# Kernel tuning notes

Hardware: AMD Instinct MI355X
Metric: run time of the kernel (lower is better)

## Reference

```python
import jax, jax.numpy as jnp
import numpy as np

NQ, NT, BSZ, E, NH = 100, 197, 128, 768, 12
HD = E // NH
EPS = 1e-12  # torch F.normalize default eps


def _l2norm(x, axis=-1):
    n = jnp.linalg.norm(x, axis=axis, keepdims=True)
    return x / jnp.maximum(n, EPS)


def setup_inputs() -> dict:
    rng = jax.random.key(0)
    ks = jax.random.split(rng, 10)
    s = 0.02  # xavier-ish scale for weights
    return {
        "query": jax.random.normal(ks[0], (NQ, BSZ, E), jnp.float32),
        "key": jax.random.normal(ks[1], (NT, BSZ, E), jnp.float32),
        "value": jax.random.normal(ks[2], (NT, BSZ, E), jnp.float32),
        "in_proj_weight": jax.random.normal(ks[3], (3 * E, E), jnp.float32) * s,
        "in_proj_bias": jnp.zeros((3 * E,), jnp.float32),
        "out_proj_weight": jax.random.normal(ks[4], (E, E), jnp.float32) * s,
        "out_proj_bias": jnp.zeros((E,), jnp.float32),
        "temperature": jnp.ones((NH, 1, 1), jnp.float32),
        "q_mapper": jax.random.normal(ks[5], (1, NT, NQ), jnp.float32),
        "x_mapper": jax.random.normal(ks[6], (1, NQ, NT), jnp.float32),
    }


def reference(query, key, value, in_proj_weight, in_proj_bias,
              out_proj_weight, out_proj_bias, temperature, q_mapper, x_mapper):
    nq, bsz, e = query.shape
    nt = key.shape[0]
    # packed in-projection: split into q/k/v weights
    wq, wk, wv = jnp.split(in_proj_weight, 3, axis=0)
    bq, bk, bv = jnp.split(in_proj_bias, 3, axis=0)
    q = query @ wq.T + bq   # [Nq, bsz, E]
    k = key @ wk.T + bk     # [Nt, bsz, E]
    v = value @ wv.T + bv   # [Nt, bsz, E]
    # reshape to [bsz, nh, hd, N] (channel-major for cross-covariance attn)
    q = q.reshape(nq, bsz, NH, HD).transpose(1, 2, 3, 0)  # [b, h, d, Nq]
    k = k.reshape(nt, bsz, NH, HD).transpose(1, 2, 3, 0)  # [b, h, d, Nt]
    v = v.reshape(nt, bsz, NH, HD).transpose(1, 2, 3, 0)  # [b, h, d, Nt]
    # normalize channel vectors over tokens
    qn = _l2norm(q)
    kn = _l2norm(k)
    # mappers: normalize over last dim, then shape to [Nq, Nt] operators
    qm_op = _l2norm(q_mapper[0])  # [Nt, Nq] normalized over Nq; transpose below
    xm_op = _l2norm(x_mapper[0])  # [Nq, Nt] normalized over Nt
    # qm = q @ q_mapper^T : [b,h,d,Nq] x [Nq,Nt] -> [b,h,d,Nt]
    qm = jnp.einsum('bhdq,tq->bhdt', qn, qm_op)
    # cross-covariance attention over channels: [b,h,d,d]
    attn = jnp.einsum('bhdt,bhet->bhde', qm, kn) * temperature[None]  # temp [nh,1,1] broadcasts per-head
    attn = jax.nn.softmax(attn, axis=-1)
    x = jnp.einsum('bhde,bhet->bhdt', attn, v)        # [b,h,d,Nt]
    out = jnp.einsum('bhdt,qt->bhdq', x, xm_op)       # [b,h,d,Nq]
    # back to [Nq, bsz, E]
    out = out.transpose(3, 0, 1, 2).reshape(nq, bsz, e)
    out = out @ out_proj_weight.T + out_proj_bias
    return out
```

## Files before the change

### kernel.cpp

```cpp
#include <hip/hip_runtime.h>
#include <hip/hip_bf16.h>

using bf16 = __hip_bfloat16;

constexpr int NQ  = 100;
constexpr int NT  = 197;
constexpr int BSZ = 128;
constexpr int EMB = 768;
constexpr int NHD = 12;
constexpr int HDD = 64;
constexpr int COLS = BSZ * EMB;
constexpr int M_Q  = 12800;
constexpr int M_KV = 25216;
constexpr int M_KVP = 25344;
constexpr int TPAD = 224;

constexpr size_t SZ_Q16  = (size_t)M_Q  * EMB * 2;
constexpr size_t SZ_KV16 = (size_t)M_KV * EMB * 2;
constexpr size_t SZ_KVP  = (size_t)M_KVP * EMB * 2;
constexpr size_t SZ_WI   = (size_t)3 * EMB * EMB * 2;
constexpr size_t SZ_T16  = (size_t)COLS * TPAD * 2;
constexpr size_t OFF_QB   = 256;
constexpr size_t OFF_KB   = OFF_QB + SZ_Q16;
constexpr size_t OFF_VB   = OFF_KB + SZ_KV16;
constexpr size_t OFF_WI   = OFF_VB + SZ_KV16;
constexpr size_t OFF_QP16 = OFF_WI + SZ_WI;
constexpr size_t OFF_KP16 = OFF_QP16 + SZ_Q16;
constexpr size_t OFF_VP16 = OFF_KP16 + SZ_KVP;
constexpr size_t OFF_QMNT = OFF_VP16 + SZ_KVP;
constexpr size_t OFF_XMNT = OFF_QMNT + 57344;
constexpr size_t OFF_WO   = OFF_XMNT + 57344;
constexpr size_t OFF_KPT  = 256;
constexpr size_t OFF_VPT  = OFF_KPT + SZ_T16;
constexpr size_t OFF_W16T = OFF_VPT + SZ_T16;
constexpr size_t OFF_QNT  = OFF_KP16;
constexpr size_t OFF_G16  = OFF_VP16;
constexpr size_t OFF_XO   = 256;

__device__ __forceinline__ float dl(const float* p) { return *p; }
__device__ __forceinline__ float dl(const bf16* p) { return __bfloat162float(*p); }

__device__ __forceinline__ ushort f2bf(float x) {
    union { float f; unsigned u; } v; v.f = x;
    unsigned r = v.u + 0x7FFFu + ((v.u >> 16) & 1u);
    return (ushort)(r >> 16);
}
__device__ __forceinline__ float bf2f(ushort x) {
    union { unsigned u; float f; } v; v.u = (unsigned)x << 16;
    return v.f;
}
__device__ __forceinline__ void dstore(float* p, float v) { *p = v; }
__device__ __forceinline__ void dstore(bf16* p, float v) { *p = __float2bfloat16(v); }

typedef __attribute__((ext_vector_type(8))) short short8;
typedef __attribute__((ext_vector_type(4))) short shortv4;
typedef __attribute__((ext_vector_type(4))) float f32x4;

__device__ __forceinline__ void gload16(const bf16* g, ushort* l) {
    __builtin_amdgcn_global_load_lds(
        (const __attribute__((address_space(1))) unsigned int*)g,
        (__attribute__((address_space(3))) unsigned int*)l, 16, 0, 0);
}

__device__ __forceinline__ int2 xcd_swz(int bx, int by, int gx, int gy) {
    const int nwg = gx * gy;
    const int L = by * gx + bx;
    const int q = nwg >> 3, r = nwg & 7;
    const int c = L & 7, i = L >> 3;
    const int wg = (c < r ? c * (q + 1) : r * (q + 1) + (c - r) * q) + i;
    return make_int2(wg % gx, wg / gx);
}

__global__ __launch_bounds__(256) void k_cvt5(
        const float* __restrict__ s0, bf16* __restrict__ d0,
        const float* __restrict__ s1, bf16* __restrict__ d1,
        const float* __restrict__ s2, bf16* __restrict__ d2,
        const float* __restrict__ s3, bf16* __restrict__ d3,
        const float* __restrict__ s4, bf16* __restrict__ d4) {
    int bk = blockIdx.x;
    const float* s; bf16* d; int lb;
    if      (bk < 864)   { s = s0; d = d0; lb = bk; }
    else if (bk < 5664)  { s = s1; d = d1; lb = bk - 864; }
    else if (bk < 15120) { s = s2; d = d2; lb = bk - 5664; }
    else if (bk < 24576) { s = s3; d = d3; lb = bk - 15120; }
    else                 { s = s4; d = d4; lb = bk - 24576; }
    size_t i = ((size_t)lb * 256 + threadIdx.x) * 8;
    float4 a = *(const float4*)(s + i), b = *(const float4*)(s + i + 4);
    short8 r;
    r[0] = (short)f2bf(a.x); r[1] = (short)f2bf(a.y); r[2] = (short)f2bf(a.z); r[3] = (short)f2bf(a.w);
    r[4] = (short)f2bf(b.x); r[5] = (short)f2bf(b.y); r[6] = (short)f2bf(b.z); r[7] = (short)f2bf(b.w);
    *(short8*)(d + i) = r;
}

template <typename T>
__global__ __launch_bounds__(128) void k_qmn(const T* qm, bf16* dstT) {
    __shared__ float red[128];
    int t = blockIdx.x, q = threadIdx.x;
    float v = (t < NT && q < NQ) ? dl(&qm[t * NQ + q]) : 0.f;
    red[q] = v * v;
    __syncthreads();
    for (int s = 64; s > 0; s >>= 1) { if (q < s) red[q] += red[q + s]; __syncthreads(); }
    float inv = 1.f / fmaxf(sqrtf(red[0]), 1e-12f);
    dstore(&dstT[(size_t)q * TPAD + t], (t < NT && q < NQ) ? v * inv : 0.f);
}

template <typename T>
__global__ __launch_bounds__(256) void k_xmn(const T* xm, bf16* dstT) {
    __shared__ float red[256];
    int q = blockIdx.x, t = threadIdx.x;
    float v = (q < NQ && t < NT) ? dl(&xm[q * NT + t]) : 0.f;
    red[t] = v * v;
    __syncthreads();
    for (int s = 128; s > 0; s >>= 1) { if (t < s) red[t] += red[t + s]; __syncthreads(); }
    float inv = 1.f / fmaxf(sqrtf(red[0]), 1e-12f);
    if (t < TPAD) dstore(&dstT[(size_t)q * TPAD + t], (q < NQ && t < NT) ? v * inv : 0.f);
}

template <int NR, int TP, int NORM>
__global__ __launch_bounds__(256) void k_trn(const bf16* __restrict__ src,
        bf16* __restrict__ dst) {
    __shared__ ushort tile[TP * 73];
    __shared__ float ssp[4][64];
    __shared__ float inv_s[64];
    const int col0 = blockIdx.x * 64;
    const int tid = threadIdx.x;
    const int c = tid & 63, tb = tid >> 6;
    float ss = 0.f;
#pragma unroll
    for (int it = 0; it < TP / 4; ++it) {
        int t = tb + it * 4;
        ushort v = 0;
        if (t < NR) v = *(const ushort*)&src[(size_t)t * COLS + col0 + c];
        tile[t * 73 + c] = v;
        if (NORM) { float f = bf2f(v); ss = fmaf(f, f, ss); }
    }
    if (NORM) {
        ssp[tb][c] = ss;
        __syncthreads();
        if (tid < 64) {
            float s = ssp[0][tid] + ssp[1][tid] + ssp[2][tid] + ssp[3][tid];
            inv_s[tid] = 1.f / fmaxf(sqrtf(s), 1e-12f);
        }
    }
    __syncthreads();
    constexpr int UPC = TP / 8;
#pragma unroll
    for (int it = 0; it < (64 * UPC) / 256; ++it) {
        int u = tid + it * 256;
        int cc = u / UPC, t0 = (u % UPC) * 8;
        float inv = NORM ? inv_s[cc] : 1.f;
        short8 s;
#pragma unroll
        for (int r = 0; r < 8; ++r) {
            ushort raw = tile[(t0 + r) * 73 + cc];
            s[r] = NORM ? (short)f2bf(bf2f(raw) * inv) : (short)raw;
        }
        *(short8*)&dst[(size_t)(col0 + cc) * TP + t0] = s;
    }
}

__global__ __launch_bounds__(256) void k_trn2(const bf16* __restrict__ kp,
        const bf16* __restrict__ vp, bf16* __restrict__ kpT, bf16* __restrict__ vpT) {
    __shared__ ushort tile[TPAD * 73];
    __shared__ float ssp[4][64];
    __shared__ float inv_s[64];
    const int bk = blockIdx.x;
    const bool vseg = bk >= 1536;
    const bf16* src = vseg ? vp : kp;
    bf16* dst = vseg ? vpT : kpT;
    const int col0 = (vseg ? bk - 1536 : bk) * 64;
    const int tid = threadIdx.x;
    const int c = tid & 63, tb = tid >> 6;
    float ss = 0.f;
#pragma unroll
    for (int it = 0; it < TPAD / 4; ++it) {
        int t = tb + it * 4;
        ushort v = 0;
        if (t < NT) v = *(const ushort*)&src[(size_t)t * COLS + col0 + c];
        tile[t * 73 + c] = v;
        if (!vseg) { float f = bf2f(v); ss = fmaf(f, f, ss); }
    }
    if (!vseg) {
        ssp[tb][c] = ss;
        __syncthreads();
        if (tid < 64) {
            float s = ssp[0][tid] + ssp[1][tid] + ssp[2][tid] + ssp[3][tid];
            inv_s[tid] = 1.f / fmaxf(sqrtf(s), 1e-12f);
        }
    }
    __syncthreads();
    constexpr int UPC = TPAD / 8;
#pragma unroll
    for (int it = 0; it < (64 * UPC) / 256; ++it) {
        int u = tid + it * 256;
        int cc = u / UPC, t0 = (u % UPC) * 8;
        float inv = vseg ? 1.f : inv_s[cc];
        short8 s;
#pragma unroll
        for (int r = 0; r < 8; ++r) {
            ushort raw = tile[(t0 + r) * 73 + cc];
            s[r] = vseg ? (short)raw : (short)f2bf(bf2f(raw) * inv);
        }
        *(short8*)&dst[(size_t)(col0 + cc) * TPAD + t0] = s;
    }
}

#define MM8_BAR  { __builtin_amdgcn_s_barrier(); __builtin_amdgcn_sched_barrier(0); }
#define MM8_LGK0 { asm volatile("s_waitcnt lgkmcnt(0)" ::: "memory"); __builtin_amdgcn_sched_barrier(0); }
#define MM8_VM8  { asm volatile("s_waitcnt vmcnt(8)" ::: "memory"); __builtin_amdgcn_sched_barrier(0); }
#define MM8_VM0  { asm volatile("s_waitcnt vmcnt(0)" ::: "memory"); __builtin_amdgcn_sched_barrier(0); }
#define MM8_STAGE(CUR, ISB, H, KT) do { \
    const bf16* gb_ = (ISB) ? (Wb + (size_t)(n0 + (H)*128 + srow) * EMB + (KT)*64 + sk_sw) \
                            : (Ab + (size_t)(m0 + (H)*128 + srow) * EMB + (KT)*64 + sk_sw); \
    ushort* lb_ = ((ISB) ? B_lds : A_lds) + (CUR)*16384 + (H)*8192 + wid*512; \
    gload16(gb_, lb_); \
    gload16(gb_ + (size_t)64 * EMB, lb_ + 4096); \
} while (0)
#define MM8_LOADFRAGS(CUR, KK, AARR, BARR) { \
    _Pragma("unroll") for (int m_ = 0; m_ < 8; ++m_) { \
        int ra_ = wr*128 + m_*16 + ln15; \
        AARR[m_] = *(const short8*)&A_lds[(CUR)*16384 + ra_*64 + ((((KK)*4 + q8) ^ (ra_ & 7)))*8]; } \
    _Pragma("unroll") for (int j_ = 0; j_ < 4; ++j_) { \
        int rb_ = wc*64 + j_*16 + ln15; \
        BARR[j_] = *(const short8*)&B_lds[(CUR)*16384 + rb_*64 + ((((KK)*4 + q8) ^ (rb_ & 7)))*8]; } }
#define MM8_QUAD(AARR, BARR, MB) { \
    __builtin_amdgcn_s_setprio(1); \
    _Pragma("unroll") for (int m_ = 0; m_ < 4; ++m_) \
        _Pragma("unroll") for (int j_ = 0; j_ < 4; ++j_) \
            acc[(MB) + m_][j_] = __builtin_amdgcn_mfma_f32_16x16x32_bf16( \
                AARR[(MB) + m_], BARR[j_], acc[(MB) + m_][j_], 0, 0, 0); \
    __builtin_amdgcn_s_setprio(0); }

__global__ __launch_bounds__(512, 2) void k_mm8(
        const bf16* __restrict__ A0, const bf16* __restrict__ A1, const bf16* __restrict__ A2,
        const bf16* __restrict__ W,
        bf16* __restrict__ C0, bf16* __restrict__ C1, bf16* __restrict__ C2,
        const float* __restrict__ bias, int mt0, int mt01) {
    __shared__ __align__(16) ushort A_lds[2 * 16384];
    __shared__ __align__(16) ushort B_lds[2 * 16384];
    const int tid = threadIdx.x;
    const int2 bxy = xcd_swz(blockIdx.x, blockIdx.y, gridDim.x, gridDim.y);
    int seg = 0, lby = bxy.y;
    if (bxy.y < mt0)       { seg = 0; lby = bxy.y; }
    else if (bxy.y < mt01) { seg = 1; lby = bxy.y - mt0; }
    else                   { seg = 2; lby = bxy.y - mt01; }
    const bf16* Ab = seg == 0 ? A0 : (seg == 1 ? A1 : A2);
    const bf16* Wb = W + (size_t)seg * EMB * EMB;
    bf16* C = seg == 0 ? C0 : (seg == 1 ? C1 : C2);
    const float* bp = bias + seg * EMB;
    const int m0 = lby * 256, n0 = bxy.x * 256;
    const int wid = tid >> 6, ln = tid & 63;
    const int wr = wid >> 2, wc = wid & 3;
    const int ln15 = ln & 15, q8 = ln >> 4;
    const int srow = tid >> 3;
    const int sk_sw = (((tid & 7) ^ (srow & 7)) * 8);

    f32x4 acc[8][4] = {};
    short8 a0[8], b0[4], a1[8], b1[4];

    MM8_STAGE(0, 0, 0, 0); MM8_STAGE(0, 0, 1, 0); MM8_STAGE(0, 1, 0, 0); MM8_STAGE(0, 1, 1, 0);
    MM8_STAGE(1, 0, 0, 1); MM8_STAGE(1, 0, 1, 1); MM8_STAGE(1, 1, 0, 1); MM8_STAGE(1, 1, 1, 1);
    MM8_VM8;
    MM8_BAR;

    for (int t = 0; t < 12; ++t) {
        const int c = t & 1, nxt = t + 2;
        MM8_LOADFRAGS(c, 0, a0, b0);
        MM8_QUAD(a0, b0, 0);
        MM8_BAR;
        MM8_LOADFRAGS(c, 1, a1, b1);
        MM8_QUAD(a0, b0, 4);
        MM8_LGK0;
        MM8_BAR;
        if (nxt < 12) { MM8_STAGE(c, 0, 0, nxt); MM8_STAGE(c, 0, 1, nxt); }
        MM8_QUAD(a1, b1, 0);
        MM8_BAR;
        if (nxt < 12) { MM8_STAGE(c, 1, 0, nxt); MM8_STAGE(c, 1, 1, nxt); }
        if (t < 10) { MM8_VM8; } else { MM8_VM0; }
        MM8_QUAD(a1, b1, 4);
        MM8_BAR;
    }

#pragma unroll
    for (int j = 0; j < 4; ++j) {
        const int n = n0 + wc * 64 + j * 16 + ln15;
        const float bv = bp[n];
#pragma unroll
        for (int m = 0; m < 8; ++m) {
            const int mb = m0 + wr * 128 + m * 16 + q8 * 4;
#pragma unroll
            for (int r = 0; r < 4; ++r)
                dstore(&C[(size_t)(mb + r) * EMB + n], acc[m][j][r] + bv);
        }
    }
}

template <typename TBias>
__global__ __launch_bounds__(256) void k_proj2(
        const bf16* __restrict__ Aq, const bf16* __restrict__ Ak, const bf16* __restrict__ Av,
        const bf16* __restrict__ Wi, bf16* __restrict__ Cq, bf16* __restrict__ Ck,
        bf16* __restrict__ Cv, const TBias* __restrict__ bias) {
    __shared__ __align__(16) ushort As[128 * 32];
    __shared__ __align__(16) ushort Bs[128 * 32];
    const int t = threadIdx.x;
    const int2 bxy = xcd_swz(blockIdx.x, blockIdx.y, gridDim.x, gridDim.y);
    int byy = bxy.y, seg, lby;
    if (byy < 100)      { seg = 0; lby = byy; }
    else if (byy < 297) { seg = 1; lby = byy - 100; }
    else                { seg = 2; lby = byy - 297; }
    const bf16* Ab = seg == 0 ? Aq : (seg == 1 ? Ak : Av);
    const bf16* Wb = Wi + (size_t)seg * EMB * EMB;
    bf16* C = seg == 0 ? Cq : (seg == 1 ? Ck : Cv);
    const TBias* bp = bias + seg * EMB;
    const int n0 = bxy.x * 128, m0 = lby * 128;
    const int ln = t & 63, wv = t >> 6;
    const int ln15 = ln & 15, q8 = ln >> 4;
    const int mw = (wv & 1) * 64, nw = (wv >> 1) * 64;
    const int sr = ln >> 2, sk = (ln & 3) * 8;
    const bf16* gA = Ab + (size_t)(m0 + wv * 32 + sr) * EMB + sk;
    const bf16* gB = Wb + (size_t)(n0 + wv * 32 + sr) * EMB + sk;
    const size_t r16 = (size_t)16 * EMB;
    ushort* lA = &As[wv * 1024];
    ushort* lB = &Bs[wv * 1024];
    f32x4 acc[4][4] = {};
    for (int k0 = 0; k0 < EMB; k0 += 32) {
        gload16(gA + k0,       lA);
        gload16(gA + r16 + k0, lA + 512);
        gload16(gB + k0,       lB);
        gload16(gB + r16 + k0, lB + 512);
        __syncthreads();
        short8 a[4], b[4];
#pragma unroll
        for (int i = 0; i < 4; ++i)
            a[i] = *(const short8*)&As[(mw + i * 16 + ln15) * 32 + q8 * 8];
#pragma unroll
        for (int j = 0; j < 4; ++j)
            b[j] = *(const short8*)&Bs[(nw + j * 16 + ln15) * 32 + q8 * 8];
#pragma unroll
        for (int i = 0; i < 4; ++i)
#pragma unroll
            for (int j = 0; j < 4; ++j)
                acc[i][j] = __builtin_amdgcn_mfma_f32_16x16x32_bf16(a[i], b[j], acc[i][j], 0, 0, 0);
        __syncthreads();
    }
#pragma unroll
    for (int j = 0; j < 4; ++j) {
        const int n = n0 + nw + j * 16 + ln15;
        const float bv = dl(&bp[n]);
#pragma unroll
        for (int i = 0; i < 4; ++i) {
            const int mb = m0 + mw + i * 16 + q8 * 4;
#pragma unroll
            for (int r = 0; r < 4; ++r)
                dstore(&C[(size_t)(mb + r) * EMB + n], acc[i][j][r] + bv);
        }
    }
}

__global__ __launch_bounds__(256) void k_gw(
        const bf16* __restrict__ kpT, const bf16* __restrict__ vpT,
        const bf16* __restrict__ qmnT, const bf16* __restrict__ xmnT,
        bf16* __restrict__ g16, bf16* __restrict__ w16T) {
    __shared__ __align__(16) ushort As[128 * 32];
    __shared__ __align__(16) ushort Bs[128 * 32];
    const int t = threadIdx.x;
    const int2 bxy = xcd_swz(blockIdx.x, blockIdx.y, gridDim.x, gridDim.y);
    const bool wseg = bxy.y >= 768;
    const int lby = wseg ? bxy.y - 768 : bxy.y;
    const bf16* Ab = wseg ? vpT : kpT;
    const bf16* Bb = wseg ? xmnT : qmnT;
    const int m0 = lby * 128;
    const int ln = t & 63, wv = t >> 6;
    const int ln15 = ln & 15, q8 = ln >> 4;
    const int mw = (wv & 1) * 64, nw = (wv >> 1) * 64;
    const int sr = ln >> 2, sk = (ln & 3) * 8;
    const bf16* gA = Ab + (size_t)(m0 + wv * 32 + sr) * TPAD + sk;
    const bf16* gB = Bb + (size_t)(wv * 32 + sr) * TPAD + sk;
    const size_t r16 = (size_t)16 * TPAD;
    ushort* lA = &As[wv * 1024];
    ushort* lB = &Bs[wv * 1024];
    f32x4 acc[4][4] = {};
    for (int k0 = 0; k0 < TPAD; k0 += 32) {
        gload16(gA + k0,       lA);
        gload16(gA + r16 + k0, lA + 512);
        gload16(gB + k0,       lB);
        gload16(gB + r16 + k0, lB + 512);
        __syncthreads();
        short8 a[4], b[4];
#pragma unroll
        for (int i = 0; i < 4; ++i)
            a[i] = *(const short8*)&As[(mw + i * 16 + ln15) * 32 + q8 * 8];
#pragma unroll
        for (int j = 0; j < 4; ++j)
            b[j] = *(const short8*)&Bs[(nw + j * 16 + ln15) * 32 + q8 * 8];
#pragma unroll
        for (int i = 0; i < 4; ++i)
#pragma unroll
            for (int j = 0; j < 4; ++j)
                acc[i][j] = __builtin_amdgcn_mfma_f32_16x16x32_bf16(a[i], b[j], acc[i][j], 0, 0, 0);
        __syncthreads();
    }
#pragma unroll
    for (int j = 0; j < 4; ++j) {
        const int n = nw + j * 16 + ln15;
#pragma unroll
        for (int i = 0; i < 4; ++i) {
            const int mb = m0 + mw + i * 16 + q8 * 4;
            if (wseg) {
                shortv4 s;
#pragma unroll
                for (int r = 0; r < 4; ++r) s[r] = (short)f2bf(acc[i][j][r]);
                *(shortv4*)&w16T[(size_t)n * COLS + mb] = s;
            } else {
#pragma unroll
                for (int r = 0; r < 4; ++r)
                    dstore(&g16[(size_t)(mb + r) * 128 + n], acc[i][j][r]);
            }
        }
    }
}

template <typename TC, typename TBias>
__global__ __launch_bounds__(256) void k_gemm_mfma(
        const bf16* __restrict__ Ab, const bf16* __restrict__ Wb,
        TC* __restrict__ C, const TBias* __restrict__ bias,
        int M, int N, int K, int ldc) {
    __shared__ __align__(16) ushort As[128 * 32];
    __shared__ __align__(16) ushort Bs[128 * 32];
    const int t = threadIdx.x;
    const int2 bxy = xcd_swz(blockIdx.x, blockIdx.y, gridDim.x, gridDim.y);
    const int n0 = bxy.x * 128, m0 = bxy.y * 128;
    const int ln = t & 63, wv = t >> 6;
    const int ln15 = ln & 15, q8 = ln >> 4;
    const int mw = (wv & 1) * 64, nw = (wv >> 1) * 64;
    const int sr = ln >> 2, sk = (ln & 3) * 8;
    const bf16* gA = Ab + (size_t)(m0 + wv * 32 + sr) * K + sk;
    const bf16* gB = Wb + (size_t)(n0 + wv * 32 + sr) * K + sk;
    const size_t r16 = (size_t)16 * K;
    ushort* lA = &As[wv * 1024];
    ushort* lB = &Bs[wv * 1024];
    f32x4 acc[4][4] = {};
    for (int k0 = 0; k0 < K; k0 += 32) {
        gload16(gA + k0,       lA);
        gload16(gA + r16 + k0, lA + 512);
        gload16(gB + k0,       lB);
        gload16(gB + r16 + k0, lB + 512);
        __syncthreads();
        short8 a[4], b[4];
#pragma unroll
        for (int i = 0; i < 4; ++i)
            a[i] = *(const short8*)&As[(mw + i * 16 + ln15) * 32 + q8 * 8];
#pragma unroll
        for (int j = 0; j < 4; ++j)
            b[j] = *(const short8*)&Bs[(nw + j * 16 + ln15) * 32 + q8 * 8];
#pragma unroll
        for (int i = 0; i < 4; ++i)
#pragma unroll
            for (int j = 0; j < 4; ++j)
                acc[i][j] = __builtin_amdgcn_mfma_f32_16x16x32_bf16(a[i], b[j], acc[i][j], 0, 0, 0);
        __syncthreads();
    }
#pragma unroll
    for (int j = 0; j < 4; ++j) {
        const int n = n0 + nw + j * 16 + ln15;
        const float bv = dl(&bias[n]);
#pragma unroll
        for (int i = 0; i < 4; ++i) {
            const int mb = m0 + mw + i * 16 + q8 * 4;
#pragma unroll
            for (int r = 0; r < 4; ++r)
                dstore(&C[(size_t)(mb + r) * ldc + n], acc[i][j][r] + bv);
        }
    }
}

template <typename T>
__global__ __launch_bounds__(256) void k_attn(
        const bf16* __restrict__ qnT, const bf16* __restrict__ g16,
        const bf16* __restrict__ w16T, const T* __restrict__ temp,
        bf16* __restrict__ xo) {
    const int h = blockIdx.x, b = blockIdx.y;
    const int tid = threadIdx.x;
    const int ln = tid & 63, wv = tid >> 6;
    const int ln15 = ln & 15, q8 = ln >> 4;
    const int colbase = b * EMB + h * HDD;
    __shared__ __align__(16) ushort smem[16384];
    char* sm = (char*)smem;

    short8 wreg[4];
#pragma unroll
    for (int it = 0; it < 4; ++it) {
        int u = tid + it * 256;
        int q = u >> 3, e0 = (u & 7) * 8;
        wreg[it] = *(const short8*)&w16T[(size_t)q * COLS + colbase + e0];
    }

#pragma unroll
    for (int it = 0; it < 4; ++it) {
        int u = tid + it * 256;
        int e = u >> 4, q0 = (u & 15) * 8;
        short8 s = *(const short8*)&g16[(size_t)(colbase + e) * 128 + q0];
        *(short8*)(sm + ((e * 256 + q0 * 2) ^ ((e & 7) << 4))) = s;
    }
#pragma unroll
    for (int it = 0; it < 4; ++it) {
        int u = tid + it * 256;
        int d = u >> 4, q0 = (u & 15) * 8;
        short8 s = *(const short8*)&qnT[(size_t)(colbase + d) * 128 + q0];
        *(short8*)(sm + 16384 + ((d * 256 + q0 * 2) ^ ((d & 7) << 4))) = s;
    }
    __syncthreads();

    const int drow = 16 * wv + ln15;
    f32x4 acc[4] = {};
#pragma unroll
    for (int ks = 0; ks < 4; ++ks) {
        short8 bfrag = *(const short8*)(sm + 16384 +
            ((drow * 256 + ks * 64 + q8 * 16) ^ ((drow & 7) << 4)));
#pragma unroll
        for (int i = 0; i < 4; ++i) {
            int erow = i * 16 + ln15;
            short8 afrag = *(const short8*)(sm +
                ((erow * 256 + ks * 64 + q8 * 16) ^ ((erow & 7) << 4)));
            acc[i] = __builtin_amdgcn_mfma_f32_16x16x32_bf16(afrag, bfrag, acc[i], 0, 0, 0);
        }
    }

    const float tv = dl(&temp[h]);
    float p[4][4];
    float mx = -1e30f;
#pragma unroll
    for (int i = 0; i < 4; ++i)
#pragma unroll
        for (int r = 0; r < 4; ++r) { p[i][r] = acc[i][r] * tv; mx = fmaxf(mx, p[i][r]); }
    mx = fmaxf(mx, __shfl_xor(mx, 16, 64));
    mx = fmaxf(mx, __shfl_xor(mx, 32, 64));
    float sum = 0.f;
#pragma unroll
    for (int i = 0; i < 4; ++i)
#pragma unroll
        for (int r = 0; r < 4; ++r) { p[i][r] = __expf(p[i][r] - mx); sum += p[i][r]; }
    sum += __shfl_xor(sum, 16, 64);
    sum += __shfl_xor(sum, 32, 64);
    const float rs = 1.f / sum;

    __syncthreads();

#pragma unroll
    for (int i = 0; i < 4; ++i) {
        shortv4 s4;
#pragma unroll
        for (int r = 0; r < 4; ++r) s4[r] = (short)f2bf(p[i][r] * rs);
        *(shortv4*)(sm + 16384 + drow * 144 + q8 * 8 + 32 * i) = s4;
    }
#pragma unroll
    for (int it = 0; it < 4; ++it) {
        int u = tid + it * 256;
        int q = u >> 3, e0 = (u & 7) * 8;
        *(short8*)(sm + ((q * 128 + e0 * 2) ^ ((q & 7) << 4))) = wreg[it];
    }
    __syncthreads();

    f32x4 o[7] = {};
#pragma unroll
    for (int ks = 0; ks < 2; ++ks) {
        short8 afrag = *(const short8*)(sm + 16384 + drow * 144 + ks * 64 + q8 * 16);
#pragma unroll
        for (int j = 0; j < 7; ++j) {
            int qrow = j * 16 + ln15;
            short8 bfrag = *(const short8*)(sm +
                ((qrow * 128 + ks * 64 + q8 * 16) ^ ((qrow & 7) << 4)));
            o[j] = __builtin_amdgcn_mfma_f32_16x16x32_bf16(afrag, bfrag, o[j], 0, 0, 0);
        }
    }
    const int dbase = h * HDD + 16 * wv + q8 * 4;
#pragma unroll
    for (int j = 0; j < 7; ++j) {
        int q = j * 16 + ln15;
        if (q < NQ) {
            shortv4 s4;
#pragma unroll
            for (int r = 0; r < 4; ++r) s4[r] = (short)f2bf(o[j][r]);
            *(shortv4*)&xo[(size_t)(q * BSZ + b) * EMB + dbase] = s4;
        }
    }
}

extern "C" void kernel_launch(void* const* d_in, const int* in_sizes, int n_in,
                              void* d_out, int out_size, void* d_ws, size_t ws_size,
                              hipStream_t stream) {
    char* ws = (char*)d_ws;
    bf16* qb16  = (bf16*)(ws + OFF_QB);
    bf16* kb16  = (bf16*)(ws + OFF_KB);
    bf16* vb16  = (bf16*)(ws + OFF_VB);
    bf16* wi16  = (bf16*)(ws + OFF_WI);
    bf16* qp16  = (bf16*)(ws + OFF_QP16);
    bf16* kp16  = (bf16*)(ws + OFF_KP16);
    bf16* vp16  = (bf16*)(ws + OFF_VP16);
    bf16* qmnT  = (bf16*)(ws + OFF_QMNT);
    bf16* xmnT  = (bf16*)(ws + OFF_XMNT);
    bf16* wo16  = (bf16*)(ws + OFF_WO);
    bf16* kpT   = (bf16*)(ws + OFF_KPT);
    bf16* vpT   = (bf16*)(ws + OFF_VPT);
    bf16* w16T  = (bf16*)(ws + OFF_W16T);
    bf16* qnT   = (bf16*)(ws + OFF_QNT);
    bf16* g16   = (bf16*)(ws + OFF_G16);
    bf16* xo16  = (bf16*)(ws + OFF_XO);

    const bool isbf = (in_sizes[0] == 19660800);

    if (isbf) {
        k_qmn<bf16><<<224, 128, 0, stream>>>((const bf16*)d_in[8], qmnT);
        k_xmn<bf16><<<128, 256, 0, stream>>>((const bf16*)d_in[9], xmnT);
        k_proj2<bf16><<<dim3(6, 494), 256, 0, stream>>>(
            (const bf16*)d_in[0], (const bf16*)d_in[1], (const bf16*)d_in[2],
            (const bf16*)d_in[3], qp16, kp16, vp16, (const bf16*)d_in[4]);
        k_trn2<<<3072, 256, 0, stream>>>(kp16, vp16, kpT, vpT);
        k_trn<NQ, 128, 1><<<COLS / 64, 256, 0, stream>>>(qp16, qnT);
        k_gw<<<dim3(1, 1536), 256, 0, stream>>>(kpT, vpT, qmnT, xmnT, g16, w16T);
        k_attn<bf16><<<dim3(NHD, BSZ), 256, 0, stream>>>(
            qnT, g16, w16T, (const bf16*)d_in[7], xo16);
        k_gemm_mfma<bf16, bf16><<<dim3(6, 100), 256, 0, stream>>>(
            xo16, (const bf16*)d_in[5], (bf16*)d_out, (const bf16*)d_in[6],
            M_Q, EMB, EMB, EMB);
    } else {
        k_qmn<float><<<224, 128, 0, stream>>>((const float*)d_in[8], qmnT);
        k_xmn<float><<<128, 256, 0, stream>>>((const float*)d_in[9], xmnT);
        k_cvt5<<<24864, 256, 0, stream>>>(
            (const float*)d_in[3], wi16,
            (const float*)d_in[0], qb16,
            (const float*)d_in[1], kb16,
            (const float*)d_in[2], vb16,
            (const float*)d_in[5], wo16);
        k_mm8<<<dim3(3, 248), 512, 0, stream>>>(
            qb16, kb16, vb16, wi16, qp16, kp16, vp16,
            (const float*)d_in[4], 50, 149);
        k_trn2<<<3072, 256, 0, stream>>>(kp16, vp16, kpT, vpT);
        k_trn<NQ, 128, 1><<<COLS / 64, 256, 0, stream>>>(qp16, qnT);
        k_gw<<<dim3(1, 1536), 256, 0, stream>>>(kpT, vpT, qmnT, xmnT, g16, w16T);
        k_attn<float><<<dim3(NHD, BSZ), 256, 0, stream>>>(
            qnT, g16, w16T, (const float*)d_in[7], xo16);
        k_gemm_mfma<float, float><<<dim3(6, 100), 256, 0, stream>>>(
            xo16, wo16, (float*)d_out, (const float*)d_in[6], M_Q, EMB, EMB, EMB);
    }
}
```

Measured before the change: 464.1 us.

## Merge mapper-normalize kernels and drop two barriers in projection GEMM loop

Merges the two small mapper-normalization kernels into one launch with a branch on block index, saving one kernel launch. Separately, removes two workgroup barriers inside the main k-loop of the in-projection MFMA GEMM so LDS fragment loads and MFMA work can overlap with staging. Dropping the barriers risks LDS read/write races between the fragment loads and the next stage writes, depending on how the double buffer is arranged.

```diff
diff --git a/kernel.cpp b/kernel.cpp
--- a/kernel.cpp
+++ b/kernel.cpp
@@ -93,27 +93,28 @@
 }
 
 template <typename T>
-__global__ __launch_bounds__(128) void k_qmn(const T* qm, bf16* dstT) {
-    __shared__ float red[128];
-    int t = blockIdx.x, q = threadIdx.x;
-    float v = (t < NT && q < NQ) ? dl(&qm[t * NQ + q]) : 0.f;
-    red[q] = v * v;
-    __syncthreads();
-    for (int s = 64; s > 0; s >>= 1) { if (q < s) red[q] += red[q + s]; __syncthreads(); }
-    float inv = 1.f / fmaxf(sqrtf(red[0]), 1e-12f);
-    dstore(&dstT[(size_t)q * TPAD + t], (t < NT && q < NQ) ? v * inv : 0.f);
-}
-
-template <typename T>
-__global__ __launch_bounds__(256) void k_xmn(const T* xm, bf16* dstT) {
+__global__ __launch_bounds__(256) void k_maps(const T* __restrict__ qm, bf16* qmnT,
+                                              const T* __restrict__ xm, bf16* xmnT) {
     __shared__ float red[256];
-    int q = blockIdx.x, t = threadIdx.x;
-    float v = (q < NQ && t < NT) ? dl(&xm[q * NT + t]) : 0.f;
-    red[t] = v * v;
-    __syncthreads();
-    for (int s = 128; s > 0; s >>= 1) { if (t < s) red[t] += red[t + s]; __syncthreads(); }
-    float inv = 1.f / fmaxf(sqrtf(red[0]), 1e-12f);
-    if (t < TPAD) dstore(&dstT[(size_t)q * TPAD + t], (q < NQ && t < NT) ? v * inv : 0.f);
+    const int bk = blockIdx.x, tid = threadIdx.x;
+    if (bk < 224) {
+        int t = bk;
+        float v = (t < NT && tid < NQ) ? dl(&qm[t * NQ + tid]) : 0.f;
+        if (tid < 128) red[tid] = v * v;
+        __syncthreads();
+        for (int s = 64; s > 0; s >>= 1) { if (tid < s) red[tid] += red[tid + s]; __syncthreads(); }
+        float inv = 1.f / fmaxf(sqrtf(red[0]), 1e-12f);
+        if (tid < 128)
+            dstore(&qmnT[(size_t)tid * TPAD + t], (t < NT && tid < NQ) ? v * inv : 0.f);
+    } else {
+        int q = bk - 224, t = tid;
+        float v = (q < NQ && t < NT) ? dl(&xm[q * NT + t]) : 0.f;
+        red[t] = v * v;
+        __syncthreads();
+        for (int s = 128; s > 0; s >>= 1) { if (t < s) red[t] += red[t + s]; __syncthreads(); }
+        float inv = 1.f / fmaxf(sqrtf(red[0]), 1e-12f);
+        if (t < TPAD) dstore(&xmnT[(size_t)q * TPAD + t], (q < NQ && t < NT) ? v * inv : 0.f);
+    }
 }
 
 template <int NR, int TP, int NORM>
@@ -267,14 +268,12 @@
         const int c = t & 1, nxt = t + 2;
         MM8_LOADFRAGS(c, 0, a0, b0);
         MM8_QUAD(a0, b0, 0);
-        MM8_BAR;
         MM8_LOADFRAGS(c, 1, a1, b1);
         MM8_QUAD(a0, b0, 4);
         MM8_LGK0;
         MM8_BAR;
         if (nxt < 12) { MM8_STAGE(c, 0, 0, nxt); MM8_STAGE(c, 0, 1, nxt); }
         MM8_QUAD(a1, b1, 0);
-        MM8_BAR;
         if (nxt < 12) { MM8_STAGE(c, 1, 0, nxt); MM8_STAGE(c, 1, 1, nxt); }
         if (t < 10) { MM8_VM8; } else { MM8_VM0; }
         MM8_QUAD(a1, b1, 4);
@@ -610,8 +609,8 @@
     const bool isbf = (in_sizes[0] == 19660800);
 
     if (isbf) {
-        k_qmn<bf16><<<224, 128, 0, stream>>>((const bf16*)d_in[8], qmnT);
-        k_xmn<bf16><<<128, 256, 0, stream>>>((const bf16*)d_in[9], xmnT);
+        k_maps<bf16><<<352, 256, 0, stream>>>((const bf16*)d_in[8], qmnT,
+                                              (const bf16*)d_in[9], xmnT);
         k_proj2<bf16><<<dim3(6, 494), 256, 0, stream>>>(
             (const bf16*)d_in[0], (const bf16*)d_in[1], (const bf16*)d_in[2],
             (const bf16*)d_in[3], qp16, kp16, vp16, (const bf16*)d_in[4]);
@@ -624,8 +623,8 @@
             xo16, (const bf16*)d_in[5], (bf16*)d_out, (const bf16*)d_in[6],
             M_Q, EMB, EMB, EMB);
     } else {
-        k_qmn<float><<<224, 128, 0, stream>>>((const float*)d_in[8], qmnT);
-        k_xmn<float><<<128, 256, 0, stream>>>((const float*)d_in[9], xmnT);
+        k_maps<float><<<352, 256, 0, stream>>>((const float*)d_in[8], qmnT,
+                                               (const float*)d_in[9], xmnT);
         k_cvt5<<<24864, 256, 0, stream>>>(
             (const float*)d_in[3], wi16,
             (const float*)d_in[0], qb16,
```

Result: no change. 459.8 us (-0.9%).
